# Optimization experiments

Measured on AMD Instinct MI355X. Metric: run time of the kernel, lower is better.

## Reference

```python
import jax, jax.numpy as jnp
import numpy as np

B, N, T, M, DIM = 4, 4096, 16, 64, 1024
HEADS, DH = 8, 64
INNER = HEADS * DH  # 512
KV = T * M          # 1024


def setup_inputs() -> dict:
    key = jax.random.key(0)
    ks = jax.random.split(key, 8)
    x = jax.random.normal(ks[0], (B, N, DIM), jnp.float32)
    media = jax.random.normal(ks[1], (B, T, M, DIM), jnp.float32)
    # sparse media markers so cumsum(text_time) stays within [0, T]
    media_locations = jax.random.uniform(ks[2], (B, N)) < (T / N)
    ln_scale = jnp.ones((DIM,), jnp.float32)
    ln_bias = jnp.zeros((DIM,), jnp.float32)
    s_in = DIM ** -0.5
    Wq = jax.random.normal(ks[3], (DIM, INNER), jnp.float32) * s_in
    Wk = jax.random.normal(ks[4], (DIM, INNER), jnp.float32) * s_in
    Wv = jax.random.normal(ks[5], (DIM, INNER), jnp.float32) * s_in
    Wo = jax.random.normal(ks[6], (INNER, DIM), jnp.float32) * (INNER ** -0.5)
    return dict(x=x, media=media, media_locations=media_locations,
                ln_scale=ln_scale, ln_bias=ln_bias, Wq=Wq, Wk=Wk, Wv=Wv, Wo=Wo)


def reference(x, media, media_locations, ln_scale, ln_bias, Wq, Wk, Wv, Wo):
    scale = DH ** -0.5
    # LayerNorm(eps=1e-5)
    mu = jnp.mean(x, axis=-1, keepdims=True)
    var = jnp.mean((x - mu) ** 2, axis=-1, keepdims=True)
    xn = (x - mu) / jnp.sqrt(var + 1e-5) * ln_scale + ln_bias

    q = xn @ Wq                                   # [b, n, inner]
    media_f = media.reshape(B, KV, DIM)           # b (t m) d
    k = media_f @ Wk                              # [b, kv, inner]
    v = media_f @ Wv

    q = q.reshape(B, N, HEADS, DH).transpose(0, 2, 1, 3) * scale  # b h n d
    k = k.reshape(B, KV, HEADS, DH).transpose(0, 2, 1, 3)         # b h kv d
    v = v.reshape(B, KV, HEADS, DH).transpose(0, 2, 1, 3)

    sim = jnp.einsum('bhid,bhjd->bhij', q, k)     # [b, h, n, kv]

    # media-location mask: each text token attends only to its immediately
    # preceding media item (only_attend_immediate_media=True -> eq)
    text_time = jnp.cumsum(media_locations.astype(jnp.int32), axis=-1)  # [b, n]
    media_time = jnp.repeat(jnp.arange(1, T + 1), M)                    # [kv]
    mask = text_time[:, None, :, None] == media_time[None, None, None, :]
    sim = jnp.where(mask, sim, -jnp.finfo(sim.dtype).max)

    attn = jax.nn.softmax(sim, axis=-1)  # stable (subtracts rowmax), same math
    # NOTE: the original's masked_fill_ of attn for media-less text tokens is a
    # no-op (return value discarded), faithfully omitted here.

    out = jnp.einsum('bhij,bhjd->bhid', attn, v)  # b h n d
    out = out.transpose(0, 2, 1, 3).reshape(B, N, INNER)
    return out @ Wo
```

## Files before the change

kernel.cpp:

```cpp
#include <hip/hip_runtime.h>

using u16 = unsigned short;
using uch = unsigned char;

typedef __bf16 bf16x8 __attribute__((ext_vector_type(8)));
typedef float f32x4 __attribute__((ext_vector_type(4)));

#define BATCH 4
#define SEQN 4096
#define TT 16
#define MM 64
#define DIM 1024
#define HEADS 8
#define DH 64
#define INNER 512
#define KVN 1024
#define NTOK (BATCH*SEQN)
#define MAXBLK 352

#define FB_WT0  1
#define FB_CVT0 2049
#define FB_LN0  6145
#define FB_GRID (FB_LN0 + NTOK)

#define OFF_XN     ((size_t)0)
#define OFF_MEDIA  ((size_t)33554432)
#define OFF_Q      ((size_t)41943040)
#define OFF_KV     ((size_t)58720256)
#define OFF_AOUT   ((size_t)67108864)
#define OFF_WQT    ((size_t)83886080)
#define OFF_WKVT   ((size_t)84934656)
#define OFF_WOT    ((size_t)87031808)
#define OFF_VSUM   ((size_t)88145920)
#define OFF_FLAGS  ((size_t)88154112)
#define OFF_VT     ((size_t)88155136)
#define OFF_NBLK   ((size_t)92350464)
#define OFF_DESC   ((size_t)92351488)

__device__ __forceinline__ u16 f2bf(float f){
  unsigned int u = __float_as_uint(f);
  u += 0x7fffu + ((u >> 16) & 1u);
  return (u16)(u >> 16);
}
__device__ __forceinline__ float bf2f(u16 b){ return __uint_as_float(((unsigned int)b) << 16); }

__device__ __forceinline__ void async16(const u16* g, void* l){
  __builtin_amdgcn_global_load_lds((__attribute__((address_space(1))) void*)(g),
                                   (__attribute__((address_space(3))) void*)(l), 16, 0, 0);
}

__device__ __forceinline__ int detect_bf16(const unsigned int* __restrict__ x){
  __shared__ int scnt;
  const int tid = threadIdx.x;
  if (tid == 0) scnt = 0;
  __syncthreads();
  int c = 0;
  #pragma unroll
  for (int t = 0; t < 4; ++t){
    unsigned int w = x[t*256 + tid];
    unsigned int e = (w >> 7) & 0xFFu;
    c += (e >= 110u && e <= 140u) ? 1 : 0;
  }
  #pragma unroll
  for (int o = 32; o > 0; o >>= 1) c += __shfl_down(c, o);
  if ((tid & 63) == 0) atomicAdd(&scnt, c);
  __syncthreads();
  return scnt > 512 ? 1 : 0;
}

__global__ __launch_bounds__(256) void front_kernel(
    const unsigned int* __restrict__ x, const uch* __restrict__ loc,
    const void* __restrict__ ln_g, const void* __restrict__ ln_b,
    const void* __restrict__ media,
    const void* __restrict__ Wq, const void* __restrict__ Wk,
    const void* __restrict__ Wv, const void* __restrict__ Wo,
    u16* __restrict__ xn, u16* __restrict__ medb,
    u16* __restrict__ WqT, u16* __restrict__ WkvT, u16* __restrict__ WoT,
    int* __restrict__ flags, float* __restrict__ vsum,
    int4* __restrict__ desc, int* __restrict__ nblk){
  const int bid = blockIdx.x, tid = threadIdx.x;

  if (bid == 0){
    __shared__ int nonzS;
    __shared__ int wsumS[4];
    __shared__ int sbound[4][19];
    __shared__ int gcnt[72];
    int bf = detect_bf16(x);
    if (tid == 0) nonzS = 0;
    if (tid < 76) sbound[tid/19][tid%19] = 4096;
    #pragma unroll
    for (int t = 0; t < 8; ++t) vsum[t*256 + tid] = 0.f;
    __syncthreads();
    int nz = 0;
    #pragma unroll
    for (int t = 0; t < 16; ++t){
      int i = t*256 + tid;
      if ((i & 3) && loc[i]) nz++;
    }
    #pragma unroll
    for (int o = 32; o > 0; o >>= 1) nz += __shfl_down(nz, o);
    if ((tid & 63) == 0) atomicAdd(&nonzS, nz);
    __syncthreads();
    const int as32 = (nonzS == 0) ? 1 : 0;
    if (tid == 0){ flags[0] = bf; flags[1] = as32; }
    const int lane = tid & 63, wl = tid >> 6;
    for (int b = 0; b < BATCH; ++b){
      int v[16];
      if (as32){
        const int4* p = (const int4*)((const int*)loc + b*SEQN + tid*16);
        #pragma unroll
        for (int j = 0; j < 4; ++j){
          int4 q = p[j];
          v[j*4+0]=q.x!=0; v[j*4+1]=q.y!=0; v[j*4+2]=q.z!=0; v[j*4+3]=q.w!=0;
        }
      } else {
        const uchar4* p = (const uchar4*)(loc + b*SEQN + tid*16);
        #pragma unroll
        for (int j = 0; j < 4; ++j){
          uchar4 q = p[j];
          v[j*4+0]=q.x!=0; v[j*4+1]=q.y!=0; v[j*4+2]=q.z!=0; v[j*4+3]=q.w!=0;
        }
      }
      int tsum = 0;
      #pragma unroll
      for (int j = 0; j < 16; ++j) tsum += v[j];
      int s = tsum;
      #pragma unroll
      for (int o = 1; o < 64; o <<= 1){ int n2 = __shfl_up(s, o); if (lane >= o) s += n2; }
      if (lane == 63) wsumS[wl] = s;
      __syncthreads();
      int base = 0;
      for (int w2 = 0; w2 < wl; ++w2) base += wsumS[w2];
      int tt = base + s - tsum;
      #pragma unroll
      for (int j = 0; j < 16; ++j){
        if (v[j]){ tt++; if (tt <= 17) sbound[b][tt] = tid*16 + j; }
      }
      __syncthreads();
    }
    if (tid < 72){
      int bb = tid/18, g = tid%18;
      int lo = (g == 0) ? 0 : sbound[bb][g];
      int hi = (g < 17) ? sbound[bb][g+1] : 4096;
      if (hi < lo) hi = lo;
      gcnt[tid] = (hi - lo + 63) >> 6;
    }
    __syncthreads();
    if (tid == 0){
      int acc = 0;
      for (int i = 0; i < 72; ++i){ int c2 = gcnt[i]; gcnt[i] = acc; acc += c2; }
      *nblk = acc;
    }
    __syncthreads();
    if (tid < 72){
      int bb = tid/18, g = tid%18;
      int lo = (g == 0) ? 0 : sbound[bb][g];
      int hi = (g < 17) ? sbound[bb][g+1] : 4096;
      if (hi < lo) hi = lo;
      int s2 = (g == 0 || g == 17) ? -1 : (g - 1);
      int n0 = gcnt[tid];
      for (int k = lo, j = 0; k < hi; k += 64, ++j){
        int4 d; d.x = bb; d.y = s2; d.z = bb*4096 + k; d.w = min(64, hi - k);
        desc[n0 + j] = d;
      }
    }
    return;
  }

  if (bid < FB_CVT0){
    const int bf = detect_bf16(x);
    __shared__ float tile[32][33];
    int id = bid - FB_WT0;
    const void* in; u16* out; int K, N, bx, by;
    if (id < 512){       in = Wq; out = WqT;  K = DIM;   N = INNER; bx = id & 15; by = id >> 4; }
    else if (id < 1024){ in = Wk; out = WkvT; K = DIM;   N = INNER; int l = id - 512;  bx = l & 15; by = l >> 4; }
    else if (id < 1536){ in = Wv; out = WkvT + (size_t)512*1024; K = DIM; N = INNER; int l = id - 1024; bx = l & 15; by = l >> 4; }
    else {               in = Wo; out = WoT;  K = INNER; N = DIM;   int l = id - 1536; bx = l & 31; by = l >> 5; }
    int n0 = bx*32, k0 = by*32;
    int tx = tid & 31, ty = tid >> 5;
    #pragma unroll
    for (int i = 0; i < 4; ++i){
      size_t idx = (size_t)(k0 + ty + i*8)*N + n0 + tx;
      tile[ty + i*8][tx] = bf ? bf2f(((const u16*)in)[idx]) : ((const float*)in)[idx];
    }
    __syncthreads();
    #pragma unroll
    for (int i = 0; i < 4; ++i)
      out[(size_t)(n0 + ty + i*8)*K + k0 + tx] = f2bf(tile[tx][ty + i*8]);
    return;
  }

  if (bid < FB_LN0){
    const int bf = detect_bf16(x);
    size_t i = (size_t)(bid - FB_CVT0)*256 + tid;
    if (bf){
      ((ushort4*)medb)[i] = ((const ushort4*)media)[i];
    } else {
      float4 t = ((const float4*)media)[i];
      ushort4 o; o.x = f2bf(t.x); o.y = f2bf(t.y); o.z = f2bf(t.z); o.w = f2bf(t.w);
      ((ushort4*)medb)[i] = o;
    }
    return;
  }

  const int bf = detect_bf16(x);
  const int row = bid - FB_LN0;
  float v[4];
  if (bf){
    ushort4 t = ((const ushort4*)((const u16*)x + (size_t)row*DIM))[tid];
    v[0]=bf2f(t.x); v[1]=bf2f(t.y); v[2]=bf2f(t.z); v[3]=bf2f(t.w);
  } else {
    float4 t = ((const float4*)((const float*)x + (size_t)row*DIM))[tid];
    v[0]=t.x; v[1]=t.y; v[2]=t.z; v[3]=t.w;
  }
  float s = v[0]+v[1]+v[2]+v[3];
  float sq = v[0]*v[0]+v[1]*v[1]+v[2]*v[2]+v[3]*v[3];
  #pragma unroll
  for (int o = 32; o > 0; o >>= 1){ s += __shfl_down(s, o); sq += __shfl_down(sq, o); }
  __shared__ float ss[4], ssq[4];
  int wid = tid >> 6, lane = tid & 63;
  if (lane == 0){ ss[wid] = s; ssq[wid] = sq; }
  __syncthreads();
  s = ss[0]+ss[1]+ss[2]+ss[3]; sq = ssq[0]+ssq[1]+ssq[2]+ssq[3];
  float mean = s * (1.f/DIM);
  float rstd = rsqrtf(sq * (1.f/DIM) - mean*mean + 1e-5f);
  float g[4], bb[4];
  if (bf){
    ushort4 t1 = ((const ushort4*)ln_g)[tid]; ushort4 t2 = ((const ushort4*)ln_b)[tid];
    g[0]=bf2f(t1.x); g[1]=bf2f(t1.y); g[2]=bf2f(t1.z); g[3]=bf2f(t1.w);
    bb[0]=bf2f(t2.x); bb[1]=bf2f(t2.y); bb[2]=bf2f(t2.z); bb[3]=bf2f(t2.w);
  } else {
    float4 t1 = ((const float4*)ln_g)[tid]; float4 t2 = ((const float4*)ln_b)[tid];
    g[0]=t1.x; g[1]=t1.y; g[2]=t1.z; g[3]=t1.w;
    bb[0]=t2.x; bb[1]=t2.y; bb[2]=t2.z; bb[3]=t2.w;
  }
  ushort4 o;
  o.x = f2bf((v[0]-mean)*rstd*g[0] + bb[0]);
  o.y = f2bf((v[1]-mean)*rstd*g[1] + bb[1]);
  o.z = f2bf((v[2]-mean)*rstd*g[2] + bb[2]);
  o.w = f2bf((v[3]-mean)*rstd*g[3] + bb[3]);
  ((ushort4*)(xn + (size_t)row*DIM))[tid] = o;
}

__device__ __forceinline__ void stage128(const u16* __restrict__ Ab, const u16* __restrict__ Bb,
                                         int K, int k0, u16* As, u16* Bs, int tid, int wid){
  #pragma unroll
  for (int t = 0; t < 4; ++t){
    int c = t*256 + tid;
    int row = c >> 3;
    int qs = (c & 7) ^ (row & 7);
    int ldsOff = (t*256 + wid*64) * 16;
    async16(Ab + (size_t)row*K + k0 + qs*8, (char*)As + ldsOff);
    async16(Bb + (size_t)row*K + k0 + qs*8, (char*)Bs + ldsOff);
  }
}

template<int MODE>
__device__ __forceinline__ void gemm128_body(const u16* __restrict__ A, const u16* __restrict__ Bt,
                        u16* __restrict__ Cp, int Nglob, int K, float alpha, int rm, int rn,
                        u16* As0, u16* As1, u16* Bs0, u16* Bs1,
                        u16* __restrict__ vtp, float* __restrict__ vsum){
  const int tid = threadIdx.x, wid = tid >> 6, lane = tid & 63;
  const int wr = wid >> 1, wc = wid & 1;
  const int lr = lane & 15, lg = lane >> 4;
  f32x4 acc[4][4] = {};
  const u16* Ab = A + (size_t)rm*128*K;
  const u16* Bb = Bt + (size_t)rn*128*K;
  const int NT = K >> 6;

  stage128(Ab, Bb, K, 0, As0, Bs0, tid, wid);
  __syncthreads();
  for (int t = 0; t < NT; ++t){
    u16* Ac = (t & 1) ? As1 : As0;
    u16* Bc = (t & 1) ? Bs1 : Bs0;
    u16* An = (t & 1) ? As0 : As1;
    u16* Bn = (t & 1) ? Bs0 : Bs1;
    if (t + 1 < NT)
      stage128(Ab, Bb, K, (t+1)*64, An, Bn, tid, wid);
    #pragma unroll
    for (int ks = 0; ks < 2; ++ks){
      bf16x8 af[4], bfr[4];
      #pragma unroll
      for (int m = 0; m < 4; ++m){
        int row = wr*64 + m*16 + lr;
        int q = (ks*4 + lg) ^ (row & 7);
        af[m] = *(const bf16x8*)((const char*)Ac + row*128 + (q << 4));
      }
      #pragma unroll
      for (int n = 0; n < 4; ++n){
        int row = wc*64 + n*16 + lr;
        int q = (ks*4 + lg) ^ (row & 7);
        bfr[n] = *(const bf16x8*)((const char*)Bc + row*128 + (q << 4));
      }
      #pragma unroll
      for (int m = 0; m < 4; ++m)
        #pragma unroll
        for (int n = 0; n < 4; ++n)
          acc[m][n] = __builtin_amdgcn_mfma_f32_16x16x32_bf16(af[m], bfr[n], acc[m][n], 0, 0, 0);
    }
    __syncthreads();
  }
  if (MODE == 2){
    const int batch = rm >> 3;
    #pragma unroll
    for (int n = 0; n < 4; ++n){
      int col = rn*128 + wc*64 + n*16 + lr;
      float psum = 0.f;
      #pragma unroll
      for (int m = 0; m < 4; ++m){
        int row0 = rm*128 + wr*64 + m*16 + lg*4;
        #pragma unroll
        for (int r = 0; r < 4; ++r){
          float v = acc[m][n][r];
          psum += v;
          int row = row0 + r;
          u16 bv = f2bf(v);
          Cp[(size_t)row*Nglob + col] = bv;
          if (col >= 512){
            int kvi = row & 1023;
            int s = kvi >> 6, rr = kvi & 63;
            vtp[((size_t)(((row >> 10)*16 + s)*512 + (col - 512)))*64 + rr] = bv;
          }
        }
      }
      if (col >= 512) atomicAdd(&vsum[batch*512 + (col - 512)], psum);
    }
  } else {
    #pragma unroll
    for (int m = 0; m < 4; ++m){
      #pragma unroll
      for (int n = 0; n < 4; ++n){
        int row0 = rm*128 + wr*64 + m*16 + lg*4;
        int col  = rn*128 + wc*64 + n*16 + lr;
        #pragma unroll
        for (int r = 0; r < 4; ++r)
          Cp[(size_t)(row0 + r)*Nglob + col] = f2bf(acc[m][n][r] * alpha);
      }
    }
  }
}

__global__ __launch_bounds__(256) void proj_kernel(
    const u16* __restrict__ xn, const u16* __restrict__ WqT, u16* __restrict__ qb,
    const u16* __restrict__ medb, const u16* __restrict__ WkvT, u16* __restrict__ kvb,
    u16* __restrict__ vtp, float* __restrict__ vsum){
  __shared__ u16 As[2][128*64];
  __shared__ u16 Bs[2][128*64];
  if (blockIdx.x < 512){
    int bid = blockIdx.x;
    int wg = (bid & 7)*64 + (bid >> 3);
    gemm128_body<0>(xn, WqT, qb, INNER, DIM, 0.125f, wg >> 2, wg & 3,
                    As[0], As[1], Bs[0], Bs[1], nullptr, nullptr);
  } else {
    int bid = blockIdx.x - 512;
    int wg = (bid & 7)*32 + (bid >> 3);
    gemm128_body<2>(medb, WkvT, kvb, 1024, DIM, 1.f, wg >> 3, wg & 7,
                    As[0], As[1], Bs[0], Bs[1], vtp, vsum);
  }
}

template<int ROWS>
__device__ __forceinline__ void g8_stage(const u16* __restrict__ src, char* dst, int K, int t,
                                         int tid, int wid){
  #pragma unroll
  for (int i = 0; i < ROWS/64; ++i){
    int s_ = i*512 + tid;
    int row_ = s_ >> 3, g_ = s_ & 7;
    async16(src + (size_t)row_*K + t*64 + ((g_ ^ (row_ & 7)) << 3),
            dst + (size_t)(i*512 + wid*64)*16);
  }
}

template<int BN, int NT, int MODE>
__device__ __forceinline__ void gemm8_body(const u16* __restrict__ A, const u16* __restrict__ Bt,
                        void* __restrict__ Cp, int Nglob, float alpha, const int* __restrict__ flags,
                        int rm, int rn, u16* sA0, u16* sA1, u16* sB0, u16* sB1){
  constexpr int K = NT*64;
  constexpr int NREP = BN/64;
  const int tid = threadIdx.x, wid = tid >> 6, lane = tid & 63;
  const int wr = wid >> 2, wc = wid & 3;
  const int lr = lane & 15, lg = lane >> 4;
  f32x4 acc[8][NREP] = {};
  const u16* Ab = A + (size_t)rm*256*K;
  const u16* Bb = Bt + (size_t)rn*BN*K;

  g8_stage<256>(Ab, (char*)sA0, K, 0, tid, wid);
  g8_stage<BN >(Bb, (char*)sB0, K, 0, tid, wid);
  __syncthreads();

  for (int t = 0; t < NT; ++t){
    u16* Acur = (t & 1) ? sA1 : sA0;
    u16* Bcur = (t & 1) ? sB1 : sB0;
    u16* Anxt = (t & 1) ? sA0 : sA1;
    u16* Bnxt = (t & 1) ? sB0 : sB1;
    bf16x8 bfr[NREP][2];
    #pragma unroll
    for (int p = 0; p < 4; ++p){
      if (p == 0 && t + 1 < NT){
        g8_stage<256>(Ab, (char*)Anxt, K, t+1, tid, wid);
        g8_stage<BN >(Bb, (char*)Bnxt, K, t+1, tid, wid);
      }
      bf16x8 af[2][2];
      #pragma unroll
      for (int i = 0; i < 2; ++i){
        int row = wr*128 + (2*p + i)*16 + lr;
        #pragma unroll
        for (int ks = 0; ks < 2; ++ks){
          int g = (ks*4 + lg) ^ (row & 7);
          af[i][ks] = *(const bf16x8*)((const char*)Acur + row*128 + g*16);
        }
      }
      if (p == 0){
        #pragma unroll
        for (int n = 0; n < NREP; ++n){
          int row = wc*(BN/4) + n*16 + lr;
          #pragma unroll
          for (int ks = 0; ks < 2; ++ks){
            int g = (ks*4 + lg) ^ (row & 7);
            bfr[n][ks] = *(const bf16x8*)((const char*)Bcur + row*128 + g*16);
          }
        }
      }
      __builtin_amdgcn_s_barrier();
      __builtin_amdgcn_s_setprio(1);
      #pragma unroll
      for (int i = 0; i < 2; ++i)
        #pragma unroll
        for (int n = 0; n < NREP; ++n)
          #pragma unroll
          for (int ks = 0; ks < 2; ++ks)
            acc[2*p + i][n] = __builtin_amdgcn_mfma_f32_16x16x32_bf16(af[i][ks], bfr[n][ks], acc[2*p + i][n], 0, 0, 0);
      __builtin_amdgcn_s_setprio(0);
      __builtin_amdgcn_s_barrier();
    }
    if (t + 1 < NT) __syncthreads();
  }

  const bool obf = flags[0] != 0;
  #pragma unroll
  for (int m = 0; m < 8; ++m){
    #pragma unroll
    for (int n = 0; n < NREP; ++n){
      int row0 = rm*256 + wr*128 + m*16 + lg*4;
      int col  = rn*BN + wc*(BN/4) + n*16 + lr;
      #pragma unroll
      for (int r = 0; r < 4; ++r){
        float v = acc[m][n][r] * alpha;
        size_t idx = (size_t)(row0 + r)*Nglob + col;
        if (obf) ((u16*)Cp)[idx] = f2bf(v);
        else     ((float*)Cp)[idx] = v;
      }
    }
  }
}

__global__ __launch_bounds__(512) void gemm8_out_kernel(const u16* __restrict__ A,
                        const u16* __restrict__ Bt, void* __restrict__ Cp,
                        const int* __restrict__ flags){
  __shared__ u16 As[2][16384];
  __shared__ u16 Bs[2][16384];
  int flat = blockIdx.x + blockIdx.y*gridDim.x;
  int wg = (flat & 7)*32 + (flat >> 3);
  int rn = wg & 3, rm = wg >> 2;
  gemm8_body<256, 8, 1>(A, Bt, Cp, DIM, 1.f, flags, rm, rn, As[0], As[1], Bs[0], Bs[1]);
}

__global__ __launch_bounds__(256) void attn2_kernel(
    const u16* __restrict__ qb, const u16* __restrict__ kvb, const u16* __restrict__ vt,
    const int* __restrict__ nblk, const int4* __restrict__ desc,
    const float* __restrict__ vsum, u16* __restrict__ aout){
  __shared__ u16 Ks[64*64];
  __shared__ u16 Vs[64*64];
  __shared__ u16 Ps[4][16*72];
  if (blockIdx.x >= *nblk) return;
  const int4 d = desc[blockIdx.x];
  const int b = d.x, s = d.y, rowStart = d.z, cnt = d.w;
  const int h = blockIdx.y;
  const int tid = threadIdx.x, w = tid >> 6, lane = tid & 63;
  if (s < 0){
    const float inv = 1.f/1024.f;
    for (int idx = tid; idx < cnt*64; idx += 256){
      int slot = idx >> 6, c = h*64 + (idx & 63);
      aout[(size_t)(rowStart + slot)*512 + c] = f2bf(vsum[b*512 + c]*inv);
    }
    return;
  }
  const int lr = lane & 15, lg = lane >> 4;
  const size_t kbase = ((size_t)(b*1024 + s*64))*1024;
  const size_t vbase = ((size_t)(b*16 + s))*512*64;
  const int myslot = w*16 + lr;
  const size_t qrow = (size_t)(rowStart + min(myslot, cnt - 1))*512;
  #pragma unroll
  for (int t = 0; t < 2; ++t){
    int ci = t*256 + tid;
    int r = ci >> 3, q = ci & 7;
    int qs = (q ^ (r & 7)) << 3;
    async16(kvb + kbase + (size_t)r*1024 + h*64 + qs, (char*)Ks + ci*16);
    async16(vt + vbase + (size_t)(h*64 + r)*64 + qs, (char*)Vs + ci*16);
  }
  __syncthreads();
  bf16x8 qa0 = *(const bf16x8*)(qb + qrow + h*64 + lg*8);
  bf16x8 qa1 = *(const bf16x8*)(qb + qrow + h*64 + 32 + lg*8);
  f32x4 sv[4] = {};
  #pragma unroll
  for (int n = 0; n < 4; ++n){
    int row = n*16 + lr;
    int sl0 = (lg) ^ (row & 7);
    int sl1 = (4 + lg) ^ (row & 7);
    bf16x8 kb0 = *(const bf16x8*)((const char*)Ks + row*128 + sl0*16);
    sv[n] = __builtin_amdgcn_mfma_f32_16x16x32_bf16(qa0, kb0, sv[n], 0, 0, 0);
    bf16x8 kb1 = *(const bf16x8*)((const char*)Ks + row*128 + sl1*16);
    sv[n] = __builtin_amdgcn_mfma_f32_16x16x32_bf16(qa1, kb1, sv[n], 0, 0, 0);
  }
  float inv[4];
  #pragma unroll
  for (int r = 0; r < 4; ++r){
    float m = fmaxf(fmaxf(sv[0][r], sv[1][r]), fmaxf(sv[2][r], sv[3][r]));
    #pragma unroll
    for (int o = 1; o < 16; o <<= 1) m = fmaxf(m, __shfl_xor(m, o));
    float s0 = 0.f;
    #pragma unroll
    for (int n = 0; n < 4; ++n){ sv[n][r] = __expf(sv[n][r] - m); s0 += sv[n][r]; }
    #pragma unroll
    for (int o = 1; o < 16; o <<= 1) s0 += __shfl_xor(s0, o);
    inv[r] = 1.f / s0;
  }
  u16* pw = &Ps[w][0];
  #pragma unroll
  for (int n = 0; n < 4; ++n)
    #pragma unroll
    for (int r = 0; r < 4; ++r)
      pw[(4*lg + r)*72 + n*16 + lr] = f2bf(sv[n][r] * inv[r]);
  bf16x8 pa0 = *(const bf16x8*)((const char*)pw + lr*144 + lg*16);
  bf16x8 pa1 = *(const bf16x8*)((const char*)pw + lr*144 + 64 + lg*16);
  f32x4 ov[4] = {};
  #pragma unroll
  for (int n = 0; n < 4; ++n){
    int row = n*16 + lr;
    int sl0 = (lg) ^ (row & 7);
    int sl1 = (4 + lg) ^ (row & 7);
    bf16x8 vb0 = *(const bf16x8*)((const char*)Vs + row*128 + sl0*16);
    ov[n] = __builtin_amdgcn_mfma_f32_16x16x32_bf16(pa0, vb0, ov[n], 0, 0, 0);
    bf16x8 vb1 = *(const bf16x8*)((const char*)Vs + row*128 + sl1*16);
    ov[n] = __builtin_amdgcn_mfma_f32_16x16x32_bf16(pa1, vb1, ov[n], 0, 0, 0);
  }
  #pragma unroll
  for (int r = 0; r < 4; ++r){
    int slot = w*16 + 4*lg + r;
    if (slot < cnt){
      size_t orow = (size_t)(rowStart + slot)*512 + h*64;
      #pragma unroll
      for (int n = 0; n < 4; ++n)
        aout[orow + n*16 + lr] = f2bf(ov[n][r]);
    }
  }
}

extern "C" void kernel_launch(void* const* d_in, const int* in_sizes, int n_in,
                              void* d_out, int out_size, void* d_ws, size_t ws_size,
                              hipStream_t stream){
  const void* x      = d_in[0];
  const void* media  = d_in[1];
  const void* mloc   = d_in[2];
  const void* ln_g   = d_in[3];
  const void* ln_b   = d_in[4];
  const void* Wq     = d_in[5];
  const void* Wk     = d_in[6];
  const void* Wv     = d_in[7];
  const void* Wo     = d_in[8];
  char* ws = (char*)d_ws;
  u16* xn    = (u16*)(ws + OFF_XN);
  u16* medb  = (u16*)(ws + OFF_MEDIA);
  u16* qb    = (u16*)(ws + OFF_Q);
  u16* kvb   = (u16*)(ws + OFF_KV);
  u16* aout  = (u16*)(ws + OFF_AOUT);
  u16* WqT   = (u16*)(ws + OFF_WQT);
  u16* WkvT  = (u16*)(ws + OFF_WKVT);
  u16* WoT   = (u16*)(ws + OFF_WOT);
  float* vsm = (float*)(ws + OFF_VSUM);
  int* flags = (int*)(ws + OFF_FLAGS);
  u16* vt    = (u16*)(ws + OFF_VT);
  int* nblk  = (int*)(ws + OFF_NBLK);
  int4* desc = (int4*)(ws + OFF_DESC);

  front_kernel<<<FB_GRID, 256, 0, stream>>>(
      (const unsigned int*)x, (const uch*)mloc, ln_g, ln_b, media,
      Wq, Wk, Wv, Wo, xn, medb, WqT, WkvT, WoT, flags, vsm, desc, nblk);

  proj_kernel<<<768, 256, 0, stream>>>(xn, WqT, qb, medb, WkvT, kvb, vt, vsm);

  attn2_kernel<<<dim3(MAXBLK, 8), 256, 0, stream>>>(qb, kvb, vt, nblk, desc, vsm, aout);

  gemm8_out_kernel<<<dim3(4, 64), 512, 0, stream>>>(aout, WoT, d_out, flags);
}
```

Measured before the change: 119.1 us.

## Replace 256x256 output GEMM with 128x128 tiles and tighten async-copy waits

The output projection drops the 512-thread 256x256-tile kernel (256 blocks) and reuses the 128x128 gemm128 body with a new MODE 1 epilogue, launching 1024 blocks of 256 threads. The aim is to fill more CUs and improve occupancy on a GEMM with small K (512). The shared gemm128 main loop also swaps __syncthreads for explicit vmcnt waits plus raw s_barrier, so the next tile's loads stay in flight while the current tile is consumed. Smaller tiles mean less operand reuse per block and more global traffic, and the hand-written waitcnt values rely on the exact number of outstanding async loads.

Measured after the change: 119.7 us. No clear change (+0.5%).

```diff
diff --git a/kernel.cpp b/kernel.cpp
--- a/kernel.cpp
+++ b/kernel.cpp
@@ -257,9 +257,10 @@
 
 template<int MODE>
 __device__ __forceinline__ void gemm128_body(const u16* __restrict__ A, const u16* __restrict__ Bt,
-                        u16* __restrict__ Cp, int Nglob, int K, float alpha, int rm, int rn,
+                        void* __restrict__ Cp, int Nglob, int K, float alpha, int rm, int rn,
                         u16* As0, u16* As1, u16* Bs0, u16* Bs1,
-                        u16* __restrict__ vtp, float* __restrict__ vsum){
+                        u16* __restrict__ vtp, float* __restrict__ vsum,
+                        const int* __restrict__ flags){
   const int tid = threadIdx.x, wid = tid >> 6, lane = tid & 63;
   const int wr = wid >> 1, wc = wid & 1;
   const int lr = lane & 15, lg = lane >> 4;
@@ -269,14 +270,19 @@
   const int NT = K >> 6;
 
   stage128(Ab, Bb, K, 0, As0, Bs0, tid, wid);
-  __syncthreads();
   for (int t = 0; t < NT; ++t){
     u16* Ac = (t & 1) ? As1 : As0;
     u16* Bc = (t & 1) ? Bs1 : Bs0;
     u16* An = (t & 1) ? As0 : As1;
     u16* Bn = (t & 1) ? Bs0 : Bs1;
-    if (t + 1 < NT)
+    if (t + 1 < NT){
       stage128(Ab, Bb, K, (t+1)*64, An, Bn, tid, wid);
+      asm volatile("s_waitcnt vmcnt(8)" ::: "memory");
+    } else {
+      asm volatile("s_waitcnt vmcnt(0)" ::: "memory");
+    }
+    __builtin_amdgcn_s_barrier();
+    __builtin_amdgcn_sched_barrier(0);
     #pragma unroll
     for (int ks = 0; ks < 2; ++ks){
       bf16x8 af[4], bfr[4];
@@ -298,7 +304,7 @@
         for (int n = 0; n < 4; ++n)
           acc[m][n] = __builtin_amdgcn_mfma_f32_16x16x32_bf16(af[m], bfr[n], acc[m][n], 0, 0, 0);
     }
-    __syncthreads();
+    __builtin_amdgcn_s_barrier();
   }
   if (MODE == 2){
     const int batch = rm >> 3;
@@ -315,7 +321,7 @@
           psum += v;
           int row = row0 + r;
           u16 bv = f2bf(v);
-          Cp[(size_t)row*Nglob + col] = bv;
+          ((u16*)Cp)[(size_t)row*Nglob + col] = bv;
           if (col >= 512){
             int kvi = row & 1023;
             int s = kvi >> 6, rr = kvi & 63;
@@ -325,6 +331,23 @@
       }
       if (col >= 512) atomicAdd(&vsum[batch*512 + (col - 512)], psum);
     }
+  } else if (MODE == 1){
+    const bool obf = flags[0] != 0;
+    #pragma unroll
+    for (int m = 0; m < 4; ++m){
+      #pragma unroll
+      for (int n = 0; n < 4; ++n){
+        int row0 = rm*128 + wr*64 + m*16 + lg*4;
+        int col  = rn*128 + wc*64 + n*16 + lr;
+        #pragma unroll
+        for (int r = 0; r < 4; ++r){
+          float v = acc[m][n][r];
+          size_t idx = (size_t)(row0 + r)*Nglob + col;
+          if (obf) ((u16*)Cp)[idx] = f2bf(v);
+          else     ((float*)Cp)[idx] = v;
+        }
+      }
+    }
   } else {
     #pragma unroll
     for (int m = 0; m < 4; ++m){
@@ -334,7 +357,7 @@
         int col  = rn*128 + wc*64 + n*16 + lr;
         #pragma unroll
         for (int r = 0; r < 4; ++r)
-          Cp[(size_t)(row0 + r)*Nglob + col] = f2bf(acc[m][n][r] * alpha);
+          ((u16*)Cp)[(size_t)(row0 + r)*Nglob + col] = f2bf(acc[m][n][r] * alpha);
       }
     }
   }
@@ -350,119 +373,24 @@
     int bid = blockIdx.x;
     int wg = (bid & 7)*64 + (bid >> 3);
     gemm128_body<0>(xn, WqT, qb, INNER, DIM, 0.125f, wg >> 2, wg & 3,
-                    As[0], As[1], Bs[0], Bs[1], nullptr, nullptr);
+                    As[0], As[1], Bs[0], Bs[1], nullptr, nullptr, nullptr);
   } else {
     int bid = blockIdx.x - 512;
     int wg = (bid & 7)*32 + (bid >> 3);
     gemm128_body<2>(medb, WkvT, kvb, 1024, DIM, 1.f, wg >> 3, wg & 7,
-                    As[0], As[1], Bs[0], Bs[1], vtp, vsum);
-  }
-}
-
-template<int ROWS>
-__device__ __forceinline__ void g8_stage(const u16* __restrict__ src, char* dst, int K, int t,
-                                         int tid, int wid){
-  #pragma unroll
-  for (int i = 0; i < ROWS/64; ++i){
-    int s_ = i*512 + tid;
-    int row_ = s_ >> 3, g_ = s_ & 7;
-    async16(src + (size_t)row_*K + t*64 + ((g_ ^ (row_ & 7)) << 3),
-            dst + (size_t)(i*512 + wid*64)*16);
-  }
-}
-
-template<int BN, int NT, int MODE>
-__device__ __forceinline__ void gemm8_body(const u16* __restrict__ A, const u16* __restrict__ Bt,
-                        void* __restrict__ Cp, int Nglob, float alpha, const int* __restrict__ flags,
-                        int rm, int rn, u16* sA0, u16* sA1, u16* sB0, u16* sB1){
-  constexpr int K = NT*64;
-  constexpr int NREP = BN/64;
-  const int tid = threadIdx.x, wid = tid >> 6, lane = tid & 63;
-  const int wr = wid >> 2, wc = wid & 3;
-  const int lr = lane & 15, lg = lane >> 4;
-  f32x4 acc[8][NREP] = {};
-  const u16* Ab = A + (size_t)rm*256*K;
-  const u16* Bb = Bt + (size_t)rn*BN*K;
-
-  g8_stage<256>(Ab, (char*)sA0, K, 0, tid, wid);
-  g8_stage<BN >(Bb, (char*)sB0, K, 0, tid, wid);
-  __syncthreads();
-
-  for (int t = 0; t < NT; ++t){
-    u16* Acur = (t & 1) ? sA1 : sA0;
-    u16* Bcur = (t & 1) ? sB1 : sB0;
-    u16* Anxt = (t & 1) ? sA0 : sA1;
-    u16* Bnxt = (t & 1) ? sB0 : sB1;
-    bf16x8 bfr[NREP][2];
-    #pragma unroll
-    for (int p = 0; p < 4; ++p){
-      if (p == 0 && t + 1 < NT){
-        g8_stage<256>(Ab, (char*)Anxt, K, t+1, tid, wid);
-        g8_stage<BN >(Bb, (char*)Bnxt, K, t+1, tid, wid);
-      }
-      bf16x8 af[2][2];
-      #pragma unroll
-      for (int i = 0; i < 2; ++i){
-        int row = wr*128 + (2*p + i)*16 + lr;
-        #pragma unroll
-        for (int ks = 0; ks < 2; ++ks){
-          int g = (ks*4 + lg) ^ (row & 7);
-          af[i][ks] = *(const bf16x8*)((const char*)Acur + row*128 + g*16);
-        }
-      }
-      if (p == 0){
-        #pragma unroll
-        for (int n = 0; n < NREP; ++n){
-          int row = wc*(BN/4) + n*16 + lr;
-          #pragma unroll
-          for (int ks = 0; ks < 2; ++ks){
-            int g = (ks*4 + lg) ^ (row & 7);
-            bfr[n][ks] = *(const bf16x8*)((const char*)Bcur + row*128 + g*16);
-          }
-        }
-      }
-      __builtin_amdgcn_s_barrier();
-      __builtin_amdgcn_s_setprio(1);
-      #pragma unroll
-      for (int i = 0; i < 2; ++i)
-        #pragma unroll
-        for (int n = 0; n < NREP; ++n)
-          #pragma unroll
-          for (int ks = 0; ks < 2; ++ks)
-            acc[2*p + i][n] = __builtin_amdgcn_mfma_f32_16x16x32_bf16(af[i][ks], bfr[n][ks], acc[2*p + i][n], 0, 0, 0);
-      __builtin_amdgcn_s_setprio(0);
-      __builtin_amdgcn_s_barrier();
-    }
-    if (t + 1 < NT) __syncthreads();
-  }
-
-  const bool obf = flags[0] != 0;
-  #pragma unroll
-  for (int m = 0; m < 8; ++m){
-    #pragma unroll
-    for (int n = 0; n < NREP; ++n){
-      int row0 = rm*256 + wr*128 + m*16 + lg*4;
-      int col  = rn*BN + wc*(BN/4) + n*16 + lr;
-      #pragma unroll
-      for (int r = 0; r < 4; ++r){
-        float v = acc[m][n][r] * alpha;
-        size_t idx = (size_t)(row0 + r)*Nglob + col;
-        if (obf) ((u16*)Cp)[idx] = f2bf(v);
-        else     ((float*)Cp)[idx] = v;
-      }
-    }
-  }
-}
-
-__global__ __launch_bounds__(512) void gemm8_out_kernel(const u16* __restrict__ A,
+                    As[0], As[1], Bs[0], Bs[1], vtp, vsum, nullptr);
+  }
+}
+
+__global__ __launch_bounds__(256) void gemm_out_kernel(const u16* __restrict__ A,
                         const u16* __restrict__ Bt, void* __restrict__ Cp,
                         const int* __restrict__ flags){
-  __shared__ u16 As[2][16384];
-  __shared__ u16 Bs[2][16384];
-  int flat = blockIdx.x + blockIdx.y*gridDim.x;
-  int wg = (flat & 7)*32 + (flat >> 3);
-  int rn = wg & 3, rm = wg >> 2;
-  gemm8_body<256, 8, 1>(A, Bt, Cp, DIM, 1.f, flags, rm, rn, As[0], As[1], Bs[0], Bs[1]);
+  __shared__ u16 As[2][128*64];
+  __shared__ u16 Bs[2][128*64];
+  int bid = blockIdx.x;
+  int wg = (bid & 7)*128 + (bid >> 3);
+  gemm128_body<1>(A, Bt, Cp, DIM, INNER, 1.f, wg >> 3, wg & 7,
+                  As[0], As[1], Bs[0], Bs[1], nullptr, nullptr, flags);
 }
 
 __global__ __launch_bounds__(256) void attn2_kernel(
@@ -591,5 +519,5 @@
 
   attn2_kernel<<<dim3(MAXBLK, 8), 256, 0, stream>>>(qb, kvb, vt, nblk, desc, vsm, aout);
 
-  gemm8_out_kernel<<<dim3(4, 64), 512, 0, stream>>>(aout, WoT, d_out, flags);
-}
+  gemm_out_kernel<<<1024, 256, 0, stream>>>(aout, WoT, d_out, flags);
+}
```
